# Optimization experiments

Hardware: AMD Instinct MI355X
Metric: run time of the kernel (lower is better)

The kernel has to match this reference:

```python
import jax, jax.numpy as jnp
import numpy as np

RADII = (3, 5, 7)      # window_levels
S, B, D = 1024, 8, 512  # seq_len, batch, feature_dim
EPS = 1e-12             # F.normalize eps


def setup_inputs() -> dict:
    key = jax.random.key(0)
    k0, k1, k2 = jax.random.split(key, 3)
    x = jax.random.normal(k0, (S, B, D), jnp.float32)          # seq-first like the torch path
    W = jax.random.normal(k1, (3, D, D), jnp.float32) / np.sqrt(D)  # 3 level linear weights
    b = jax.random.normal(k2, (3, D), jnp.float32) * 0.01           # 3 level linear biases
    alphas = jnp.ones((3,), jnp.float32)   # nn.Parameter(torch.ones)
    betas = jnp.zeros((3,), jnp.float32)   # nn.Parameter(torch.zeros)
    return {"x": x, "W": W, "b": b, "alphas": alphas, "betas": betas}


def reference(x, W, b, alphas, betas):
    # x: [S, B, D] (seq-first). torch code transposes to [B, S, D], works, transposes back.
    # Dropout is identity (eval mode). output = x + sum over levels of per-timestep
    # windowed, similarity-weighted sums of linearly transformed neighbors; all
    # windows read the ORIGINAL x, so levels are independent additive terms.
    xb = jnp.transpose(x, (1, 0, 2))  # [B, S, D]
    Bn, Sn, Dn = xb.shape
    dt = xb.dtype
    # L2-normalized features (F.normalize with eps=1e-12)
    xnorm = xb / jnp.maximum(jnp.linalg.norm(xb, axis=-1, keepdims=True), EPS)
    # prefix sums for O(1) window means (edge-truncated windows)
    csum = jnp.concatenate([jnp.zeros((Bn, 1, Dn), dt), jnp.cumsum(xb, axis=1)], axis=1)
    t_idx = jnp.arange(Sn)
    out = xb
    for m, r in enumerate(RADII):
        starts = jnp.clip(t_idx - r, 0, Sn)        # [S]
        ends = jnp.clip(t_idx + r + 1, 0, Sn)      # [S]
        cnt = (ends - starts).astype(dt)           # window sizes (truncated at edges)
        center = (csum[:, ends, :] - csum[:, starts, :]) / cnt[None, :, None]  # [B,S,D]
        cnorm = center / jnp.maximum(jnp.linalg.norm(center, axis=-1, keepdims=True), EPS)
        # sliding-window gather indices, masked at sequence edges
        offs = jnp.arange(-r, r + 1)
        pos = t_idx[:, None] + offs[None, :]       # [S, w]
        valid = ((pos >= 0) & (pos < Sn)).astype(dt)
        idx = jnp.clip(pos, 0, Sn - 1)
        nw = xnorm[:, idx, :]                      # [B, S, w, D]
        sim = jnp.einsum('bswd,bsd->bsw', nw, cnorm)  # cosine similarity to window mean
        wts = jax.nn.sigmoid(alphas[m] * sim + betas[m]) * valid[None, :, :]
        tfm = xb @ W[m].T + b[m]                   # level-m linear transform, computed once
        tw = tfm[:, idx, :]                        # [B, S, w, D]
        out = out + jnp.einsum('bsw,bswd->bsd', wts, tw)
    return jnp.transpose(out, (1, 0, 2))  # back to [S, B, D]
```

## Files before the change

### kernel.cpp

```cpp
#include <hip/hip_runtime.h>

typedef __attribute__((ext_vector_type(8))) short short8;
typedef __attribute__((ext_vector_type(4))) float f32x4;

#define S_LEN 1024
#define B_N 8
#define D_DIM 512
#define SLAB 4194304
#define NX   4194304

static __device__ __forceinline__ unsigned short f2bf(float f){
  unsigned int u = __float_as_uint(f);
  u = u + 0x7fffu + ((u>>16)&1u);
  return (unsigned short)(u>>16);
}
static __device__ __forceinline__ float bf2f(unsigned short h){
  return __uint_as_float(((unsigned int)h)<<16);
}

#define GLL16(g,l) __builtin_amdgcn_global_load_lds( \
    (__attribute__((address_space(1))) void*)(g), \
    (__attribute__((address_space(3))) void*)(l), 16, 0, 0)

#define SBAR() do { __builtin_amdgcn_sched_barrier(0); \
  asm volatile("s_barrier" ::: "memory"); \
  __builtin_amdgcn_sched_barrier(0); } while(0)
#define VMCNT(n) asm volatile("s_waitcnt vmcnt(" #n ")" ::: "memory")

__global__ __launch_bounds__(256) void k_conv(const float* __restrict__ x,
    const float* __restrict__ W, unsigned short* __restrict__ xbf,
    unsigned short* __restrict__ wbf)
{
  size_t i = ((size_t)blockIdx.x*256 + threadIdx.x)*4;
  const float* src; unsigned short* dst;
  if (i < NX){ src = x + i; dst = xbf + i; }
  else       { src = W + (i - NX); dst = wbf + (i - NX); }
  float4 v = *(const float4*)src;
  ushort4 h;
  h.x = f2bf(v.x); h.y = f2bf(v.y); h.z = f2bf(v.z); h.w = f2bf(v.w);
  *(ushort4*)dst = h;
}

__global__ __launch_bounds__(256) void k_heavy(const unsigned short* __restrict__ A,
    const unsigned short* __restrict__ Bw, const float* __restrict__ bias,
    unsigned short* __restrict__ C, float* __restrict__ Gband)
{
  __shared__ __align__(16) unsigned short smem[24576];
  int blk = blockIdx.x;
  int tid = threadIdx.x, lane = tid & 63, w = tid >> 6;

  if (blk >= 768){
    if (w >= 3) return;
    int g = blk - 768;
    int b = g & 7, i0 = (g >> 3) * 16;
    int j0 = i0 + (w - 1) * 16;
    if (j0 < 0 || j0 >= S_LEN) return;
    int l15 = lane & 15, klo = (lane >> 4) * 8;
    const unsigned short* Ar = A + ((size_t)(i0 + l15) * B_N + b) * D_DIM + klo;
    const unsigned short* Br = A + ((size_t)(j0 + l15) * B_N + b) * D_DIM + klo;
    f32x4 acc = (f32x4){0.f,0.f,0.f,0.f};
    #pragma unroll
    for (int kt = 0; kt < 16; ++kt){
      short8 af = *(const short8*)(Ar + kt*32);
      short8 bf = *(const short8*)(Br + kt*32);
      acc = __builtin_amdgcn_mfma_f32_16x16x32_bf16(af, bf, acc, 0,0,0);
    }
    int rb = (lane >> 4) * 4;
    #pragma unroll
    for (int rg = 0; rg < 4; ++rg){
      int i = i0 + rb + rg;
      int dl = j0 + l15 - i;
      if (dl >= -14 && dl <= 14)
        Gband[((size_t)b * S_LEN + i) * 32 + dl + 14] = acc[rg];
    }
    return;
  }

  int xcd = blk & 7, ixc = blk >> 3;
  int by = xcd * 8 + ixc / 12;
  int bx = ixc % 12;
  int wm = w >> 1, wn = w & 1;
  int c0 = w*128 + lane, c1 = c0 + 64;
  const unsigned short* gA0 = A + (size_t)(by*128 + (c0>>2))*512 + (c0&3)*8;
  const unsigned short* gA1 = A + (size_t)(by*128 + (c1>>2))*512 + (c1&3)*8;
  const unsigned short* gB0 = Bw + (size_t)(bx*128 + (c0>>2))*512 + (c0&3)*8;
  const unsigned short* gB1 = Bw + (size_t)(bx*128 + (c1>>2))*512 + (c1&3)*8;
  f32x4 acc[4][4];
  #pragma unroll
  for (int i=0;i<4;++i)
    #pragma unroll
    for (int j=0;j<4;++j)
      acc[i][j] = (f32x4){0.f,0.f,0.f,0.f};
  int l15 = lane & 15, klo = (lane>>4)*8;
  {
    unsigned short* s0 = smem + w*1024;
    GLL16(gA0, s0); GLL16(gA1, s0 + 512);
    GLL16(gB0, s0 + 4096); GLL16(gB1, s0 + 4096 + 512);
    gA0 += 32; gA1 += 32; gB0 += 32; gB1 += 32;
    unsigned short* s1 = smem + 8192 + w*1024;
    GLL16(gA0, s1); GLL16(gA1, s1 + 512);
    GLL16(gB0, s1 + 4096); GLL16(gB1, s1 + 4096 + 512);
    gA0 += 32; gA1 += 32; gB0 += 32; gB1 += 32;
  }
  VMCNT(4); SBAR();
  #pragma unroll
  for (int kt = 0; kt < 16; ++kt){
    unsigned short* sc = smem + (kt % 3)*8192;
    if (kt + 2 < 16){
      unsigned short* sn = smem + ((kt + 2) % 3)*8192 + w*1024;
      GLL16(gA0, sn); GLL16(gA1, sn + 512);
      GLL16(gB0, sn + 4096); GLL16(gB1, sn + 4096 + 512);
      gA0 += 32; gA1 += 32; gB0 += 32; gB1 += 32;
    }
    short8 af[4], bfr[4];
    #pragma unroll
    for (int i=0;i<4;++i)
      af[i] = *(const short8*)(sc + (wm*64 + i*16 + l15)*32 + klo);
    #pragma unroll
    for (int j=0;j<4;++j)
      bfr[j] = *(const short8*)(sc + 4096 + (wn*64 + j*16 + l15)*32 + klo);
    #pragma unroll
    for (int i=0;i<4;++i)
      #pragma unroll
      for (int j=0;j<4;++j)
        acc[i][j] = __builtin_amdgcn_mfma_f32_16x16x32_bf16(af[i], bfr[j], acc[i][j], 0,0,0);
    if (kt < 15){
      __builtin_amdgcn_sched_barrier(0);
      if (kt + 2 < 16){ VMCNT(4); }
      else            { VMCNT(0); }
      SBAR();
    }
  }
  __syncthreads();
  int rbase = (lane>>4)*4;
  #pragma unroll
  for (int j=0;j<4;++j){
    int nl = wn*64 + j*16 + l15;
    float bv = bias[bx*128 + nl];
    #pragma unroll
    for (int i=0;i<4;++i){
      int rl0 = wm*64 + i*16 + rbase;
      #pragma unroll
      for (int rg=0;rg<4;++rg)
        smem[(rl0+rg)*128 + nl] = f2bf(acc[i][j][rg] + bv);
    }
  }
  __syncthreads();
  int m_r = bx >> 2, colb = (bx&3)*128;
  #pragma unroll
  for (int p=0;p<8;++p){
    int R = p*16 + (tid>>4);
    int ch = (tid&15)*8;
    uint4 v = *(const uint4*)(smem + R*128 + ch);
    *(uint4*)(C + (size_t)m_r*SLAB + (size_t)(by*128 + R)*512 + colb + ch) = v;
  }
}

__global__ __launch_bounds__(256) void k_gath(const float* __restrict__ x,
    const unsigned short* __restrict__ tfm, const float* __restrict__ Gband,
    const float* __restrict__ alphas, const float* __restrict__ betas,
    float* __restrict__ out)
{
  int blk = blockIdx.x;
  int b = blk & 7, tg = blk >> 3;
  int tid = threadIdx.x, h = tid >> 7, j = tid & 127;
  int t = tg * 2 + h;
  __shared__ float pshare[2][33];
  __shared__ float invc[2][3];
  __shared__ float wsh[2][33];
  int m = 0, pos = 0, valid = 0;
  float pp = 0.f, invnp = 0.f;
  if (j < 33){
    int r, wsl;
    if (j < 7){ m = 0; r = 3; wsl = j; }
    else if (j < 18){ m = 1; r = 5; wsl = j - 7; }
    else { m = 2; r = 7; wsl = j - 18; }
    pos = t + wsl - r;
    valid = (pos >= 0 && pos < S_LEN);
    if (valid){
      const float* grow = Gband + ((size_t)b * S_LEN + pos) * 32;
      int ulo = max(t - r, 0), uhi = min(t + r, S_LEN - 1);
      for (int u = ulo; u <= uhi; ++u) pp += grow[u - pos + 14];
      invnp = rsqrtf(fmaxf(grow[14], 1e-24f));
    }
    pshare[h][j] = valid ? pp : 0.f;
  }
  __syncthreads();
  if (j < 3){
    int s0 = j == 0 ? 0 : (j == 1 ? 7 : 18);
    int c  = j == 0 ? 7 : (j == 1 ? 11 : 15);
    float s = 0.f;
    for (int k = 0; k < c; ++k) s += pshare[h][s0 + k];
    invc[h][j] = rsqrtf(fmaxf(s, 1e-24f));
  }
  __syncthreads();
  if (j < 33){
    float wt = 0.f;
    if (valid){
      float sim = pp * invnp * invc[h][m];
      float z = alphas[m] * sim + betas[m];
      wt = 1.0f / (1.0f + expf(-z));
    }
    wsh[h][j] = wt;
  }
  __syncthreads();
  int d0 = j * 4;
  size_t xoff = ((size_t)t * B_N + b) * D_DIM + d0;
  float4 a = *(const float4*)(x + xoff);
  float ax = a.x, ay = a.y, az = a.z, aw = a.w;
  #pragma unroll
  for (int p = 0; p < 33; ++p){
    int pm, pr, wsl;
    if (p < 7){ pm = 0; pr = 3; wsl = p; }
    else if (p < 18){ pm = 1; pr = 5; wsl = p - 7; }
    else { pm = 2; pr = 7; wsl = p - 18; }
    int ppos = t + wsl - pr;
    if (ppos < 0 || ppos >= S_LEN) continue;
    float wt = wsh[h][p];
    const unsigned short* tp = tfm + (size_t)pm * SLAB + ((size_t)ppos * B_N + b) * D_DIM + d0;
    uint2 uv = *(const uint2*)tp;
    ax += wt * bf2f((unsigned short)(uv.x & 0xffffu));
    ay += wt * bf2f((unsigned short)(uv.x >> 16));
    az += wt * bf2f((unsigned short)(uv.y & 0xffffu));
    aw += wt * bf2f((unsigned short)(uv.y >> 16));
  }
  *(float4*)(out + xoff) = make_float4(ax, ay, az, aw);
}

extern "C" void kernel_launch(void* const* d_in, const int* in_sizes, int n_in,
                              void* d_out, int out_size, void* d_ws, size_t ws_size,
                              hipStream_t stream) {
  const float* x      = (const float*)d_in[0];
  const float* W      = (const float*)d_in[1];
  const float* bias   = (const float*)d_in[2];
  const float* alphas = (const float*)d_in[3];
  const float* betas  = (const float*)d_in[4];
  float* out = (float*)d_out;
  char* ws = (char*)d_ws;
  unsigned short* xbf  = (unsigned short*)ws;
  unsigned short* wbf  = (unsigned short*)(ws + 8388608);
  unsigned short* tfm  = (unsigned short*)(ws + 8388608 + 1572864);
  float*          Gband= (float*)(ws + 8388608 + 1572864 + 25165824);

  k_conv <<<4864, 256, 0, stream>>>(x, W, xbf, wbf);
  k_heavy<<<1280, 256, 0, stream>>>(xbf, wbf, bias, tfm, Gband);
  k_gath <<<4096, 256, 0, stream>>>(x, tfm, Gband, alphas, betas, out);
}
```

Baseline: 63.39 us.

## Move Gram-band computation into conversion kernel reading fp32 x directly

The banded Gram blocks (neighbor dot products) move out of the GEMM kernel into the bf16 conversion kernel as extra blocks. They now load fp32 x and convert it in registers, so they no longer depend on the converted buffer. The GEMM launch shrinks to only its 768 tiles, which removes the tail imbalance from mixing the two block types. Separately, the gather kernel issues its x load before the weight-computation barriers so that load latency overlaps them. The band blocks now read twice the bytes of fp32 input and add conversion work inside the memory-bound conversion kernel.

```diff
diff --git a/kernel.cpp b/kernel.cpp
--- a/kernel.cpp
+++ b/kernel.cpp
@@ -27,55 +27,63 @@
   __builtin_amdgcn_sched_barrier(0); } while(0)
 #define VMCNT(n) asm volatile("s_waitcnt vmcnt(" #n ")" ::: "memory")
 
-__global__ __launch_bounds__(256) void k_conv(const float* __restrict__ x,
+__global__ __launch_bounds__(256) void k_pre(const float* __restrict__ x,
     const float* __restrict__ W, unsigned short* __restrict__ xbf,
-    unsigned short* __restrict__ wbf)
+    unsigned short* __restrict__ wbf, float* __restrict__ Gband)
 {
-  size_t i = ((size_t)blockIdx.x*256 + threadIdx.x)*4;
-  const float* src; unsigned short* dst;
-  if (i < NX){ src = x + i; dst = xbf + i; }
-  else       { src = W + (i - NX); dst = wbf + (i - NX); }
-  float4 v = *(const float4*)src;
-  ushort4 h;
-  h.x = f2bf(v.x); h.y = f2bf(v.y); h.z = f2bf(v.z); h.w = f2bf(v.w);
-  *(ushort4*)dst = h;
+  int blk = blockIdx.x;
+  int tid = threadIdx.x;
+  if (blk < 4864){
+    size_t i = ((size_t)blk*256 + tid)*4;
+    const float* src; unsigned short* dst;
+    if (i < NX){ src = x + i; dst = xbf + i; }
+    else       { src = W + (i - NX); dst = wbf + (i - NX); }
+    float4 v = *(const float4*)src;
+    ushort4 h;
+    h.x = f2bf(v.x); h.y = f2bf(v.y); h.z = f2bf(v.z); h.w = f2bf(v.w);
+    *(ushort4*)dst = h;
+    return;
+  }
+  int lane = tid & 63, w = tid >> 6;
+  if (w >= 3) return;
+  int g = blk - 4864;
+  int b = g & 7, i0 = (g >> 3) * 16;
+  int j0 = i0 + (w - 1) * 16;
+  if (j0 < 0 || j0 >= S_LEN) return;
+  int l15 = lane & 15, klo = (lane >> 4) * 8;
+  const float* Ar = x + ((size_t)(i0 + l15) * B_N + b) * D_DIM + klo;
+  const float* Br = x + ((size_t)(j0 + l15) * B_N + b) * D_DIM + klo;
+  f32x4 acc = (f32x4){0.f,0.f,0.f,0.f};
+  #pragma unroll
+  for (int kt = 0; kt < 16; ++kt){
+    float4 a0 = *(const float4*)(Ar + kt*32);
+    float4 a1 = *(const float4*)(Ar + kt*32 + 4);
+    float4 b0 = *(const float4*)(Br + kt*32);
+    float4 b1 = *(const float4*)(Br + kt*32 + 4);
+    short8 af, bf;
+    af[0]=f2bf(a0.x); af[1]=f2bf(a0.y); af[2]=f2bf(a0.z); af[3]=f2bf(a0.w);
+    af[4]=f2bf(a1.x); af[5]=f2bf(a1.y); af[6]=f2bf(a1.z); af[7]=f2bf(a1.w);
+    bf[0]=f2bf(b0.x); bf[1]=f2bf(b0.y); bf[2]=f2bf(b0.z); bf[3]=f2bf(b0.w);
+    bf[4]=f2bf(b1.x); bf[5]=f2bf(b1.y); bf[6]=f2bf(b1.z); bf[7]=f2bf(b1.w);
+    acc = __builtin_amdgcn_mfma_f32_16x16x32_bf16(af, bf, acc, 0,0,0);
+  }
+  int rb = (lane >> 4) * 4;
+  #pragma unroll
+  for (int rg = 0; rg < 4; ++rg){
+    int i = i0 + rb + rg;
+    int dl = j0 + l15 - i;
+    if (dl >= -14 && dl <= 14)
+      Gband[((size_t)b * S_LEN + i) * 32 + dl + 14] = acc[rg];
+  }
 }
 
 __global__ __launch_bounds__(256) void k_heavy(const unsigned short* __restrict__ A,
     const unsigned short* __restrict__ Bw, const float* __restrict__ bias,
-    unsigned short* __restrict__ C, float* __restrict__ Gband)
+    unsigned short* __restrict__ C)
 {
   __shared__ __align__(16) unsigned short smem[24576];
   int blk = blockIdx.x;
   int tid = threadIdx.x, lane = tid & 63, w = tid >> 6;
-
-  if (blk >= 768){
-    if (w >= 3) return;
-    int g = blk - 768;
-    int b = g & 7, i0 = (g >> 3) * 16;
-    int j0 = i0 + (w - 1) * 16;
-    if (j0 < 0 || j0 >= S_LEN) return;
-    int l15 = lane & 15, klo = (lane >> 4) * 8;
-    const unsigned short* Ar = A + ((size_t)(i0 + l15) * B_N + b) * D_DIM + klo;
-    const unsigned short* Br = A + ((size_t)(j0 + l15) * B_N + b) * D_DIM + klo;
-    f32x4 acc = (f32x4){0.f,0.f,0.f,0.f};
-    #pragma unroll
-    for (int kt = 0; kt < 16; ++kt){
-      short8 af = *(const short8*)(Ar + kt*32);
-      short8 bf = *(const short8*)(Br + kt*32);
-      acc = __builtin_amdgcn_mfma_f32_16x16x32_bf16(af, bf, acc, 0,0,0);
-    }
-    int rb = (lane >> 4) * 4;
-    #pragma unroll
-    for (int rg = 0; rg < 4; ++rg){
-      int i = i0 + rb + rg;
-      int dl = j0 + l15 - i;
-      if (dl >= -14 && dl <= 14)
-        Gband[((size_t)b * S_LEN + i) * 32 + dl + 14] = acc[rg];
-    }
-    return;
-  }
-
   int xcd = blk & 7, ixc = blk >> 3;
   int by = xcd * 8 + ixc / 12;
   int bx = ixc % 12;
@@ -165,6 +173,9 @@
   int b = blk & 7, tg = blk >> 3;
   int tid = threadIdx.x, h = tid >> 7, j = tid & 127;
   int t = tg * 2 + h;
+  int d0 = j * 4;
+  size_t xoff = ((size_t)t * B_N + b) * D_DIM + d0;
+  float4 a = *(const float4*)(x + xoff);
   __shared__ float pshare[2][33];
   __shared__ float invc[2][3];
   __shared__ float wsh[2][33];
@@ -204,9 +215,6 @@
     wsh[h][j] = wt;
   }
   __syncthreads();
-  int d0 = j * 4;
-  size_t xoff = ((size_t)t * B_N + b) * D_DIM + d0;
-  float4 a = *(const float4*)(x + xoff);
   float ax = a.x, ay = a.y, az = a.z, aw = a.w;
   #pragma unroll
   for (int p = 0; p < 33; ++p){
@@ -242,7 +250,7 @@
   unsigned short* tfm  = (unsigned short*)(ws + 8388608 + 1572864);
   float*          Gband= (float*)(ws + 8388608 + 1572864 + 25165824);
 
-  k_conv <<<4864, 256, 0, stream>>>(x, W, xbf, wbf);
-  k_heavy<<<1280, 256, 0, stream>>>(xbf, wbf, bias, tfm, Gband);
+  k_pre  <<<5376, 256, 0, stream>>>(x, W, xbf, wbf, Gband);
+  k_heavy<<< 768, 256, 0, stream>>>(xbf, wbf, bias, tfm);
   k_gath <<<4096, 256, 0, stream>>>(x, tfm, Gband, alphas, betas, out);
 }
```

New measurement: 92.38 us. 45.7% more time.
